# Performance work log

Hardware: AMD Instinct MI355X
Metric: run time of the kernel (lower is better)

The kernel has to match this reference:

```python
import jax, jax.numpy as jnp
import numpy as np

HEADS = 2
NEG_SLOPE = 0.2

def _seg_softmax(alpha, dst, n):
    # numerically-stable softmax over edges grouped by destination node (PyG softmax)
    m = jax.ops.segment_max(alpha, dst, num_segments=n)
    m = jax.lax.stop_gradient(jnp.where(jnp.isfinite(m), m, 0.0))
    e = jnp.exp(alpha - m[dst])
    s = jax.ops.segment_sum(e, dst, num_segments=n)
    return e / (s[dst] + 1e-16)

def _han_layer(xo, xa, e_oo, e_oa, e_ao, Wo, bo, Wa, ba, asrc, adst, Wk, bk, q):
    No, Na = xo.shape[0], xa.shape[0]
    C = Wo.shape[1]
    D = C // HEADS
    h = {'object': (xo @ Wo + bo).reshape(No, HEADS, D),
         'attribute': (xa @ Wa + ba).reshape(Na, HEADS, D)}
    n = {'object': No, 'attribute': Na}
    edge_types = [('object', 'object', e_oo), ('object', 'attribute', e_oa),
                  ('attribute', 'object', e_ao)]
    outs = {'object': [], 'attribute': []}
    for i, (st, dt, e) in enumerate(edge_types):
        src, dst = e[0], e[1]
        # per-edge attention logits [E, H]
        a = (h[st] * asrc[i]).sum(-1)[src] + (h[dt] * adst[i]).sum(-1)[dst]
        a = jax.nn.leaky_relu(a, NEG_SLOPE)
        a = _seg_softmax(a, dst, n[dt])
        msg = (h[st][src] * a[..., None]).reshape(-1, C)  # [E, C]
        outs[dt].append(jax.nn.relu(jax.ops.segment_sum(msg, dst, num_segments=n[dt])))
    res = {}
    for nt, xs in outs.items():
        o = jnp.stack(xs)  # [M, N, C] over metapaths
        score = (q * jnp.tanh(o @ Wk + bk).mean(axis=1)).sum(-1)  # [M]
        w = jax.nn.softmax(score, axis=0)
        res[nt] = jnp.einsum('m,mnc->nc', w, o)
    return res


def setup_inputs() -> dict:
    key = jax.random.key(0)
    ks = jax.random.split(key, 40)
    No, Na, E, C, H = 100000, 50000, 500000, 128, 2
    D = C // H
    def rn(k, shape, scale):
        return jax.random.normal(k, shape, jnp.float32) * scale
    inp = {}
    inp['x_object'] = rn(ks[0], (No, C), 1.0)
    inp['x_attribute'] = rn(ks[1], (Na, C), 1.0)
    inp['e_oo'] = jax.random.randint(ks[2], (2, E), 0, No)
    inp['e_oa'] = jnp.stack([jax.random.randint(ks[3], (E,), 0, No),
                             jax.random.randint(ks[4], (E,), 0, Na)])
    inp['e_ao'] = jnp.stack([jax.random.randint(ks[5], (E,), 0, Na),
                             jax.random.randint(ks[6], (E,), 0, No)])
    s = 1.0 / float(np.sqrt(C))
    for L, off in (('1', 7), ('2', 16)):
        inp['Wo' + L] = rn(ks[off], (C, C), s)
        inp['bo' + L] = jnp.zeros((C,), jnp.float32)
        inp['Wa' + L] = rn(ks[off + 1], (C, C), s)
        inp['ba' + L] = jnp.zeros((C,), jnp.float32)
        inp['asrc' + L] = rn(ks[off + 2], (3, H, D), s)
        inp['adst' + L] = rn(ks[off + 3], (3, H, D), s)
        inp['Wk' + L] = rn(ks[off + 4], (C, C), s)
        inp['bk' + L] = jnp.zeros((C,), jnp.float32)
        inp['q' + L] = rn(ks[off + 5], (C,), s)
    inp['Wl1'] = rn(ks[30], (C, 256), s)
    inp['bl1'] = jnp.zeros((256,), jnp.float32)
    inp['Wl2'] = rn(ks[31], (256, 128), 1.0 / float(np.sqrt(256)))
    inp['bl2'] = jnp.zeros((128,), jnp.float32)
    inp['Wl3'] = rn(ks[32], (128, 8), 1.0 / float(np.sqrt(128)))
    inp['bl3'] = jnp.zeros((8,), jnp.float32)
    return inp


def reference(x_object, x_attribute, e_oo, e_oa, e_ao,
              Wo1, bo1, Wa1, ba1, asrc1, adst1, Wk1, bk1, q1,
              Wo2, bo2, Wa2, ba2, asrc2, adst2, Wk2, bk2, q2,
              Wl1, bl1, Wl2, bl2, Wl3, bl3):
    h = _han_layer(x_object, x_attribute, e_oo, e_oa, e_ao,
                   Wo1, bo1, Wa1, ba1, asrc1, adst1, Wk1, bk1, q1)
    h = _han_layer(h['object'], h['attribute'], e_oo, e_oa, e_ao,
                   Wo2, bo2, Wa2, ba2, asrc2, adst2, Wk2, bk2, q2)
    x = h['object'] @ Wl1 + bl1
    x = x @ Wl2 + bl2
    x = x @ Wl3 + bl3
    return jax.nn.sigmoid(x)
```

## Files before the change

kernel.cpp:

```cpp
#include <hip/hip_runtime.h>
#include <hip/hip_bf16.h>
#include <math.h>

#define CDIM 128
typedef unsigned short u16;
typedef unsigned int u32;
typedef short bf16x8 __attribute__((ext_vector_type(8)));
typedef float f32x4 __attribute__((ext_vector_type(4)));

__device__ __forceinline__ float bf2f(__hip_bfloat16 h) { return __bfloat162float(h); }
__device__ __forceinline__ u16 f2bfbits(float f) {
  __hip_bfloat16 h = __float2bfloat16(f);
  u16 u;
  __builtin_memcpy(&u, &h, 2);
  return u;
}
__device__ __forceinline__ float bfbits2f(u16 b) { return __uint_as_float((u32)b << 16); }
__device__ __forceinline__ float lrelu(float v) { return v > 0.f ? v : 0.2f * v; }
__device__ __forceinline__ float lo_bf(u32 v) { return __uint_as_float(v << 16); }
__device__ __forceinline__ float hi_bf(u32 v) { return __uint_as_float(v & 0xffff0000u); }
__device__ __forceinline__ u32 pack_bf(float a, float b) {
  return (u32)f2bfbits(a) | ((u32)f2bfbits(b) << 16);
}

__global__ void detect_kernel(const u16* __restrict__ p, int nwords, int* __restrict__ flag) {
  int i = blockIdx.x * blockDim.x + threadIdx.x;
  if (i >= nwords) return;
  int ex = (p[i] >> 7) & 0xFF;
  if (ex >= 0xC0) atomicOr(flag, 1);
}

struct CvtJob { const void* src; float* dst; int n; };
struct CvtJobs24 { CvtJob j[24]; };
__global__ void cvt_batch_kernel(CvtJobs24 jobs, const int* __restrict__ flag) {
  CvtJob jb = jobs.j[blockIdx.y];
  int i = blockIdx.x * blockDim.x + threadIdx.x;
  if (i >= jb.n) return;
  if (*flag) jb.dst[i] = ((const float*)jb.src)[i];
  else jb.dst[i] = bf2f(((const __hip_bfloat16*)jb.src)[i]);
}

__global__ void fill_out_kernel(void* __restrict__ out, float v, int n,
                                const int* __restrict__ flag) {
  int i = blockIdx.x * blockDim.x + threadIdx.x;
  if (i >= n) return;
  if (*flag) ((float*)out)[i] = v;
  else ((__hip_bfloat16*)out)[i] = __float2bfloat16(v);
}

struct RepackJobs { const float* src[6]; u16* dst[6]; };
__global__ void repack_w_kernel(RepackJobs jobs) {
  const float* W = jobs.src[blockIdx.y];
  u16* Wf = jobs.dst[blockIdx.y];
  int idx = blockIdx.x * 256 + threadIdx.x;
  int j = idx & 7, lane = (idx >> 3) & 63, kc = (idx >> 9) & 3, nt = idx >> 11;
  int k = kc * 32 + ((lane >> 4) & 3) * 8 + j;
  int n = nt * 16 + (lane & 15);
  Wf[idx] = f2bfbits(W[k * 128 + n]);
}

struct CsrJobs {
  const int* src[3]; const int* dst[3];
  int* deg[3]; int* cur[3]; int* bsum[3]; int* offs[3]; int* adj[3];
  int Nd[3]; int E;
};
__global__ void deg_batch_kernel(CsrJobs c) {
  int y = blockIdx.y;
  int e = blockIdx.x * blockDim.x + threadIdx.x;
  if (e < c.E) atomicAdd(&c.deg[y][c.dst[y][e]], 1);
}
__global__ void scanp_batch_kernel(CsrJobs c) {
  int y = blockIdx.y, N = c.Nd[y];
  __shared__ int red[256];
  int t = threadIdx.x;
  int base = blockIdx.x * 1024 + t * 4;
  int s = 0;
#pragma unroll
  for (int j = 0; j < 4; ++j) if (base + j < N) s += c.deg[y][base + j];
  red[t] = s;
  __syncthreads();
  for (int o = 128; o; o >>= 1) {
    if (t < o) red[t] += red[t + o];
    __syncthreads();
  }
  if (t == 0) c.bsum[y][blockIdx.x] = red[0];
}
__global__ void scanb_batch_kernel(CsrJobs c) {
  int y = threadIdx.x;
  if (y >= 3) return;
  int nb = (c.Nd[y] + 1023) / 1024;
  int run = 0;
  for (int i = 0; i < nb; ++i) { int v = c.bsum[y][i]; c.bsum[y][i] = run; run += v; }
  c.offs[y][c.Nd[y]] = c.E;
}
__global__ void scanf_batch_kernel(CsrJobs c) {
  int y = blockIdx.y, N = c.Nd[y];
  __shared__ int lds[256];
  int t = threadIdx.x;
  int base = blockIdx.x * 1024 + t * 4;
  int v0 = (base + 0 < N) ? c.deg[y][base + 0] : 0;
  int v1 = (base + 1 < N) ? c.deg[y][base + 1] : 0;
  int v2 = (base + 2 < N) ? c.deg[y][base + 2] : 0;
  int v3 = (base + 3 < N) ? c.deg[y][base + 3] : 0;
  int tsum = v0 + v1 + v2 + v3;
  lds[t] = tsum;
  __syncthreads();
  for (int o = 1; o < 256; o <<= 1) {
    int x = (t >= o) ? lds[t - o] : 0;
    __syncthreads();
    lds[t] += x;
    __syncthreads();
  }
  int excl = lds[t] - tsum + c.bsum[y][blockIdx.x];
  int e0 = excl, e1 = excl + v0, e2 = excl + v0 + v1, e3 = excl + v0 + v1 + v2;
  if (base + 0 < N) { c.offs[y][base + 0] = e0; c.cur[y][base + 0] = e0; }
  if (base + 1 < N) { c.offs[y][base + 1] = e1; c.cur[y][base + 1] = e1; }
  if (base + 2 < N) { c.offs[y][base + 2] = e2; c.cur[y][base + 2] = e2; }
  if (base + 3 < N) { c.offs[y][base + 3] = e3; c.cur[y][base + 3] = e3; }
}
__global__ void fill_batch_kernel(CsrJobs c, int R) {
  int y = blockIdx.y;
  int e = blockIdx.x * blockDim.x + threadIdx.x;
  if (e >= c.E) return;
  int Nd = c.Nd[y];
  int range = (Nd + R - 1) / R;
  int lo = blockIdx.z * range;
  int d = c.dst[y][e];
  if (d < lo || d >= lo + range) return;
  int p = atomicAdd(&c.cur[y][d], 1);
  c.adj[y][p] = c.src[y][e];
}

struct GemmJob {
  const void* X; const void* X2; const float* W2;
  const u16* Wf; const float* bias;
  const float* av[4]; float* od[4]; int K;
  u16* out; int M; int mode;
};
struct GemmJobs2 { GemmJob j[2]; };
__global__ __launch_bounds__(256, 4) void gemm_mfma_kernel(
    GemmJobs2 g, const int* __restrict__ flag, int nb0)
{
  int jbi = ((int)blockIdx.x >= nb0) ? 1 : 0;
  GemmJob jb = g.j[jbi];
  int bx = jbi ? (int)blockIdx.x - nb0 : (int)blockIdx.x;
  int M = jb.M;
  __shared__ u16 Cs[64][136];
  int wave = threadIdx.x >> 6, lane = threadIdx.x & 63;
  int row0 = bx * 64 + wave * 16;
  int m = lane & 15, ko = (lane >> 4) * 8, rq = lane >> 4;
  bool wact = row0 < M;
  if (wact) {
    int r = row0 + m; if (r >= M) r = M - 1;
    bf16x8 a[4];
    if (jb.mode == 1 && *flag) {
      const float* af = (const float*)jb.X + (size_t)r * 128 + ko;
#pragma unroll
      for (int c = 0; c < 4; ++c) {
        float4 x = *(const float4*)(af + c * 32);
        float4 y = *(const float4*)(af + c * 32 + 4);
        bf16x8 tv;
        tv[0] = (short)f2bfbits(x.x); tv[1] = (short)f2bfbits(x.y);
        tv[2] = (short)f2bfbits(x.z); tv[3] = (short)f2bfbits(x.w);
        tv[4] = (short)f2bfbits(y.x); tv[5] = (short)f2bfbits(y.y);
        tv[6] = (short)f2bfbits(y.z); tv[7] = (short)f2bfbits(y.w);
        a[c] = tv;
      }
    } else if (jb.mode == 2) {
      float w0 = jb.W2[0], w1 = jb.W2[1];
      const u16* g1 = (const u16*)jb.X + (size_t)r * 128 + ko;
      const u16* g2 = (const u16*)jb.X2 + (size_t)r * 128 + ko;
#pragma unroll
      for (int c = 0; c < 4; ++c) {
        bf16x8 x1 = *(const bf16x8*)(g1 + c * 32);
        bf16x8 x2 = *(const bf16x8*)(g2 + c * 32);
        bf16x8 tv;
#pragma unroll
        for (int k = 0; k < 8; ++k)
          tv[k] = (short)f2bfbits(w0 * bfbits2f((u16)x1[k]) + w1 * bfbits2f((u16)x2[k]));
        a[c] = tv;
      }
    } else {
      const u16* ab = (const u16*)jb.X + (size_t)r * 128 + ko;
#pragma unroll
      for (int c = 0; c < 4; ++c) a[c] = *(const bf16x8*)(ab + c * 32);
    }
    f32x4 acc[8];
#pragma unroll
    for (int nt = 0; nt < 8; ++nt) acc[nt] = (f32x4){0.f, 0.f, 0.f, 0.f};
#pragma unroll
    for (int c = 0; c < 4; ++c) {
      bf16x8 b[8];
#pragma unroll
      for (int nt = 0; nt < 8; ++nt)
        b[nt] = *(const bf16x8*)(jb.Wf + ((nt * 4 + c) * 64 + lane) * 8);
#pragma unroll
      for (int nt = 0; nt < 8; ++nt)
        acc[nt] = __builtin_amdgcn_mfma_f32_16x16x32_bf16(a[c], b[nt], acc[nt], 0, 0, 0);
    }
#pragma unroll
    for (int nt = 0; nt < 8; ++nt) {
      float bv = jb.bias[nt * 16 + m];
#pragma unroll
      for (int reg = 0; reg < 4; ++reg) acc[nt][reg] += bv;
    }
#pragma unroll
    for (int nt = 0; nt < 8; ++nt) {
      int col = nt * 16 + m;
#pragma unroll
      for (int reg = 0; reg < 4; ++reg)
        Cs[wave * 16 + rq * 4 + reg][col] = f2bfbits(acc[nt][reg]);
    }
    for (int k = 0; k < jb.K; ++k) {
      const float* avk = jb.av[k];
      float* odk = jb.od[k];
      float am[8];
#pragma unroll
      for (int nt = 0; nt < 8; ++nt) am[nt] = avk[nt * 16 + m];
#pragma unroll
      for (int reg = 0; reg < 4; ++reg) {
        float p0 = 0.f, p1 = 0.f;
#pragma unroll
        for (int nt = 0; nt < 4; ++nt) p0 = fmaf(acc[nt][reg], am[nt], p0);
#pragma unroll
        for (int nt = 4; nt < 8; ++nt) p1 = fmaf(acc[nt][reg], am[nt], p1);
#pragma unroll
        for (int msk = 1; msk < 16; msk <<= 1) {
          p0 += __shfl_xor(p0, msk);
          p1 += __shfl_xor(p1, msk);
        }
        if (m == 0) {
          int row = row0 + rq * 4 + reg;
          if (row < M) { odk[row * 2] = p0; odk[row * 2 + 1] = p1; }
        }
      }
    }
  }
  __syncthreads();
  int t = threadIdx.x;
#pragma unroll
  for (int kk = 0; kk < 4; ++kk) {
    int idx = t + kk * 256;
    int rowl = idx >> 4, c16 = idx & 15;
    int grow = bx * 64 + rowl;
    if (grow < M) {
      uint4 v = *(const uint4*)&Cs[rowl][c16 * 8];
      *(uint4*)((u16*)jb.out + (size_t)grow * 128 + c16 * 8) = v;
    }
  }
}

__global__ __launch_bounds__(256) void tanhsum_mfma_kernel(
    const u16* __restrict__ A0, const u16* __restrict__ A1,
    const u16* __restrict__ Wf, const float* __restrict__ bias,
    float* __restrict__ score, int M)
{
  const u16* A = blockIdx.y ? A1 : A0;
  float* sc = score + blockIdx.y * 128;
  __shared__ float sred[4][128];
  int wave = threadIdx.x >> 6, lane = threadIdx.x & 63;
  int m = lane & 15, ko = (lane >> 4) * 8, rq = lane >> 4;
  float colsum[8];
#pragma unroll
  for (int nt = 0; nt < 8; ++nt) colsum[nt] = 0.f;
  for (int row0 = blockIdx.x * 64 + wave * 16; row0 < M; row0 += gridDim.x * 64) {
    int r = row0 + m; if (r >= M) r = M - 1;
    const u16* arow = A + (size_t)r * 128 + ko;
    bf16x8 a[4];
#pragma unroll
    for (int c = 0; c < 4; ++c) a[c] = *(const bf16x8*)(arow + c * 32);
    f32x4 acc[8];
#pragma unroll
    for (int nt = 0; nt < 8; ++nt) acc[nt] = (f32x4){0.f, 0.f, 0.f, 0.f};
#pragma unroll
    for (int c = 0; c < 4; ++c) {
#pragma unroll
      for (int nt = 0; nt < 8; ++nt) {
        bf16x8 b = *(const bf16x8*)(Wf + ((nt * 4 + c) * 64 + lane) * 8);
        acc[nt] = __builtin_amdgcn_mfma_f32_16x16x32_bf16(a[c], b, acc[nt], 0, 0, 0);
      }
    }
#pragma unroll
    for (int nt = 0; nt < 8; ++nt) {
      float bv = bias[nt * 16 + m];
#pragma unroll
      for (int reg = 0; reg < 4; ++reg) {
        int row = row0 + rq * 4 + reg;
        if (row < M) colsum[nt] += tanhf(acc[nt][reg] + bv);
      }
    }
  }
#pragma unroll
  for (int nt = 0; nt < 8; ++nt) {
    colsum[nt] += __shfl_xor(colsum[nt], 16);
    colsum[nt] += __shfl_xor(colsum[nt], 32);
  }
  if (lane < 16) {
#pragma unroll
    for (int nt = 0; nt < 8; ++nt) sred[wave][nt * 16 + lane] = colsum[nt];
  }
  __syncthreads();
  int t = threadIdx.x;
  if (t < 128) {
    float tot = sred[0][t] + sred[1][t] + sred[2][t] + sred[3][t];
    atomicAdd(&sc[t], tot);
  }
}

__global__ void sem_w_kernel(const float* __restrict__ score, const float* __restrict__ q,
                             float invN, float* __restrict__ W2) {
  int t = threadIdx.x;
  float s0 = 0.f, s1 = 0.f;
  for (int c = t; c < 128; c += 64) {
    float qc = q[c];
    s0 += qc * score[c];
    s1 += qc * score[128 + c];
  }
#pragma unroll
  for (int o = 32; o; o >>= 1) {
    s0 += __shfl_xor(s0, o);
    s1 += __shfl_xor(s1, o);
  }
  if (t == 0) {
    s0 *= invN; s1 *= invN;
    float mx = fmaxf(s0, s1);
    float e0 = expf(s0 - mx), e1 = expf(s1 - mx);
    float inv = 1.f / (e0 + e1);
    W2[0] = e0 * inv;
    W2[1] = e1 * inv;
  }
}

struct GatherJob {
  const int* offs; const int* adj;
  const float* ss; const float* sd;
  float* ew;
  const u16* Hs; u16* out; int Nd;
};
struct GatherJobs3 { GatherJob j[3]; };
__global__ __launch_bounds__(256) void node_gather_b_kernel(GatherJobs3 g, int nb0, int nb01)
{
  int bx = blockIdx.x;
  int jbi = bx < nb0 ? 0 : (bx < nb01 ? 1 : 2);
  int bl = jbi == 0 ? bx : (jbi == 1 ? bx - nb0 : bx - nb01);
  GatherJob jb = g.j[jbi];
  int lane = threadIdx.x & 63;
  int grp = lane >> 4, sl = lane & 15;
  int wid = bl * 4 + (threadIdx.x >> 6);
  int node = wid * 4 + grp;
  bool act = node < jb.Nd;
  int beg = 0, end = 0;
  float2 sdp = make_float2(0.f, 0.f);
  if (act) {
    beg = jb.offs[node];
    end = jb.offs[node + 1];
    sdp = ((const float2*)jb.sd)[node];
  }
  int deg = end - beg;
  const float2* ss2 = (const float2*)jb.ss;
  float2* ew2 = (float2*)jb.ew;
  const uint4* H4 = (const uint4*)jb.Hs;
  bool hi2 = sl >= 8;
  int base = grp * 16;
  float a[8];
#pragma unroll
  for (int j = 0; j < 8; ++j) a[j] = 0.f;
  float invh;
  if (__all(deg <= 16)) {
    int adjreg = 0;
    if (sl < deg) adjreg = jb.adj[beg + sl];
    int sidx[8];
#pragma unroll
    for (int j = 0; j < 8; ++j) sidx[j] = __shfl(adjreg, base + j);
    float2 ssp = make_float2(0.f, 0.f);
    if (sl < deg) ssp = ss2[adjreg];
    uint4 v[8];
#pragma unroll
    for (int j = 0; j < 8; ++j)
      if (j < deg) v[j] = H4[(size_t)sidx[j] * 16 + sl];
    float e0r = 0.f, e1r = 0.f;
    if (sl < deg) {
      e0r = expf(lrelu(ssp.x + sdp.x));
      e1r = expf(lrelu(ssp.y + sdp.y));
    }
    float s0 = e0r, s1 = e1r;
#pragma unroll
    for (int o = 1; o < 16; o <<= 1) {
      s0 += __shfl_xor(s0, o);
      s1 += __shfl_xor(s1, o);
    }
    invh = 1.f / ((hi2 ? s1 : s0) + 1e-16f);
#pragma unroll
    for (int j = 0; j < 8; ++j) {
      float wl = __shfl(e0r, base + j);
      float wh = __shfl(e1r, base + j);
      if (j < deg) {
        float w = hi2 ? wh : wl;
        a[0] = fmaf(lo_bf(v[j].x), w, a[0]);
        a[1] = fmaf(hi_bf(v[j].x), w, a[1]);
        a[2] = fmaf(lo_bf(v[j].y), w, a[2]);
        a[3] = fmaf(hi_bf(v[j].y), w, a[3]);
        a[4] = fmaf(lo_bf(v[j].z), w, a[4]);
        a[5] = fmaf(hi_bf(v[j].z), w, a[5]);
        a[6] = fmaf(lo_bf(v[j].w), w, a[6]);
        a[7] = fmaf(hi_bf(v[j].w), w, a[7]);
      }
    }
    if (__any(deg > 8)) {
#pragma unroll
      for (int j = 0; j < 8; ++j) {
        int s2 = __shfl(adjreg, base + 8 + j);
        float wl = __shfl(e0r, base + 8 + j);
        float wh = __shfl(e1r, base + 8 + j);
        if (8 + j < deg) {
          uint4 vv = H4[(size_t)s2 * 16 + sl];
          float w = hi2 ? wh : wl;
          a[0] = fmaf(lo_bf(vv.x), w, a[0]);
          a[1] = fmaf(hi_bf(vv.x), w, a[1]);
          a[2] = fmaf(lo_bf(vv.y), w, a[2]);
          a[3] = fmaf(hi_bf(vv.y), w, a[3]);
          a[4] = fmaf(lo_bf(vv.z), w, a[4]);
          a[5] = fmaf(hi_bf(vv.z), w, a[5]);
          a[6] = fmaf(lo_bf(vv.w), w, a[6]);
          a[7] = fmaf(hi_bf(vv.w), w, a[7]);
        }
      }
    }
  } else {
    float s0 = 0.f, s1 = 0.f;
    for (int e = beg + sl; e < end; e += 16) {
      int s = jb.adj[e];
      float2 ssp = ss2[s];
      float f0 = expf(lrelu(ssp.x + sdp.x));
      float f1 = expf(lrelu(ssp.y + sdp.y));
      ew2[e] = make_float2(f0, f1);
      s0 += f0;
      s1 += f1;
    }
#pragma unroll
    for (int o = 1; o < 16; o <<= 1) {
      s0 += __shfl_xor(s0, o);
      s1 += __shfl_xor(s1, o);
    }
    invh = 1.f / ((hi2 ? s1 : s0) + 1e-16f);
    for (int eb = beg; eb < end; eb += 4) {
      int eA[4]; uint4 v[4]; float w[4];
#pragma unroll
      for (int j = 0; j < 4; ++j) eA[j] = (eb + j < end) ? eb + j : end - 1;
#pragma unroll
      for (int j = 0; j < 4; ++j) v[j] = H4[(size_t)jb.adj[eA[j]] * 16 + sl];
#pragma unroll
      for (int j = 0; j < 4; ++j) {
        float2 p = ew2[eA[j]];
        w[j] = (eb + j < end) ? (hi2 ? p.y : p.x) : 0.f;
      }
#pragma unroll
      for (int j = 0; j < 4; ++j) {
        a[0] = fmaf(lo_bf(v[j].x), w[j], a[0]);
        a[1] = fmaf(hi_bf(v[j].x), w[j], a[1]);
        a[2] = fmaf(lo_bf(v[j].y), w[j], a[2]);
        a[3] = fmaf(hi_bf(v[j].y), w[j], a[3]);
        a[4] = fmaf(lo_bf(v[j].z), w[j], a[4]);
        a[5] = fmaf(hi_bf(v[j].z), w[j], a[5]);
        a[6] = fmaf(lo_bf(v[j].w), w[j], a[6]);
        a[7] = fmaf(hi_bf(v[j].w), w[j], a[7]);
      }
    }
  }
  if (act) {
    uint4 o;
    o.x = pack_bf(fmaxf(a[0] * invh, 0.f), fmaxf(a[1] * invh, 0.f));
    o.y = pack_bf(fmaxf(a[2] * invh, 0.f), fmaxf(a[3] * invh, 0.f));
    o.z = pack_bf(fmaxf(a[4] * invh, 0.f), fmaxf(a[5] * invh, 0.f));
    o.w = pack_bf(fmaxf(a[6] * invh, 0.f), fmaxf(a[7] * invh, 0.f));
    ((uint4*)jb.out)[(size_t)node * 16 + sl] = o;
  }
}

__global__ void fold1_kernel(const float* __restrict__ Wl1, const float* __restrict__ bl1,
                             const float* __restrict__ Wl2, const float* __restrict__ bl2,
                             float* __restrict__ WT1, float* __restrict__ TB) {
  int idx = blockIdx.x * blockDim.x + threadIdx.x;
  if (idx < 128 * 128) {
    int m = idx >> 7, n = idx & 127;
    float acc = 0.f;
    for (int k = 0; k < 256; ++k) acc = fmaf(Wl1[m * 256 + k], Wl2[k * 128 + n], acc);
    WT1[idx] = acc;
  } else if (idx < 128 * 128 + 128) {
    int n = idx - 128 * 128;
    float acc = bl2[n];
    for (int k = 0; k < 256; ++k) acc = fmaf(bl1[k], Wl2[k * 128 + n], acc);
    TB[n] = acc;
  }
}
__global__ void fold2_kernel(const float* __restrict__ WT1, const float* __restrict__ TB,
                             const float* __restrict__ Wl3, const float* __restrict__ bl3,
                             float* __restrict__ WC, float* __restrict__ BC) {
  int idx = blockIdx.x * blockDim.x + threadIdx.x;
  if (idx < 128 * 8) {
    int m = idx >> 3, j = idx & 7;
    float acc = 0.f;
    for (int k = 0; k < 128; ++k) acc = fmaf(WT1[m * 128 + k], Wl3[k * 8 + j], acc);
    WC[idx] = acc;
  } else if (idx < 128 * 8 + 8) {
    int j = idx - 128 * 8;
    float acc = bl3[j];
    for (int k = 0; k < 128; ++k) acc = fmaf(TB[k], Wl3[k * 8 + j], acc);
    BC[j] = acc;
  }
}

__global__ __launch_bounds__(256) void final_mlp_kernel(
    const u16* __restrict__ X1, const u16* __restrict__ X2,
    const float* __restrict__ W2, const int* __restrict__ flag,
    const float* __restrict__ Wc, const float* __restrict__ bc,
    void* __restrict__ out, int M) {
  __shared__ float Xs[32][130];
  int rb = blockIdx.x * 32;
  int t = threadIdx.x;
  float w0 = W2[0], w1 = W2[1];
  for (int i = t; i < 32 * 64; i += 256) {
    int r = i >> 6, c2 = i & 63;
    int gr = rb + r;
    u32 v1 = 0, v2 = 0;
    if (gr < M) {
      v1 = ((const u32*)X1)[(size_t)gr * 64 + c2];
      v2 = ((const u32*)X2)[(size_t)gr * 64 + c2];
    }
    Xs[r][c2 * 2] = w0 * lo_bf(v1) + w1 * lo_bf(v2);
    Xs[r][c2 * 2 + 1] = w0 * hi_bf(v1) + w1 * hi_bf(v2);
  }
  __syncthreads();
  int r = t >> 3, j = t & 7;
  int gr = rb + r;
  if (gr >= M) return;
  float acc = bc[j];
#pragma unroll 4
  for (int c = 0; c < 128; ++c) acc = fmaf(Xs[r][c], Wc[c * 8 + j], acc);
  float v = 1.f / (1.f + expf(-acc));
  if (*flag) ((float*)out)[(size_t)gr * 8 + j] = v;
  else ((__hip_bfloat16*)out)[(size_t)gr * 8 + j] = __float2bfloat16(v);
}

extern "C" void kernel_launch(void* const* d_in, const int* in_sizes, int n_in,
                              void* d_out, int out_size, void* d_ws, size_t ws_size,
                              hipStream_t stream) {
  const int No = in_sizes[0] / CDIM;
  const int Na = in_sizes[1] / CDIM;
  const int E = in_sizes[2] / 2;
  const int NM = No > Na ? No : Na;

  char* base = (char*)d_ws;
  size_t off = 0;
  auto alloc = [&](size_t bytes) -> void* {
    off = (off + 255) & ~(size_t)255;
    void* p = base + off;
    off += bytes;
    return p;
  };

  int* FLAG = (int*)alloc(4);
  u16* G1b = (u16*)alloc((size_t)No * CDIM * 2);
  u16* XAb = (u16*)alloc((size_t)Na * CDIM * 2);
  u16* HOb = (u16*)alloc((size_t)No * CDIM * 2);
  u16* HAb = (u16*)alloc((size_t)Na * CDIM * 2);
  u16* G2b = (u16*)alloc((size_t)No * CDIM * 2);
  float* OD0 = (float*)alloc((size_t)No * 2 * 4);
  float* OD1 = (float*)alloc((size_t)No * 2 * 4);
  float* OD2 = (float*)alloc((size_t)No * 2 * 4);
  float* OD3 = (float*)alloc((size_t)No * 2 * 4);
  float* AD0 = (float*)alloc((size_t)Na * 2 * 4);
  float* AD1 = (float*)alloc((size_t)Na * 2 * 4);
  float* EW0 = (float*)alloc((size_t)E * 2 * 4);
  float* EW1 = (float*)alloc((size_t)E * 2 * 4);
  float* EW2 = (float*)alloc((size_t)E * 2 * 4);
  int* DEG3 = (int*)alloc((size_t)NM * 3 * 4);
  float* SCORE = (float*)alloc(512 * 4);
  float* SEMW = (float*)alloc(4 * 4);
  float* WT1 = (float*)alloc(128 * 128 * 4);
  float* TB = (float*)alloc(128 * 4);
  float* WC = (float*)alloc(128 * 8 * 4);
  float* BC = (float*)alloc(8 * 4);
  int* OFFS_OO = (int*)alloc((size_t)(No + 1) * 4);
  int* OFFS_OA = (int*)alloc((size_t)(Na + 1) * 4);
  int* OFFS_AO = (int*)alloc((size_t)(No + 1) * 4);
  int* ADJ_OO = (int*)alloc((size_t)E * 4);
  int* ADJ_OA = (int*)alloc((size_t)E * 4);
  int* ADJ_AO = (int*)alloc((size_t)E * 4);
  int* CUR3 = (int*)alloc((size_t)NM * 3 * 4);
  int* BSUM3 = (int*)alloc(3 * 128 * 4);
  u16* WF[6];
  for (int i = 0; i < 6; ++i) WF[i] = (u16*)alloc(16384 * 2);
  float* F[29];
  for (int i = 5; i < 29; ++i) F[i] = (float*)alloc((size_t)in_sizes[i] * 4);

  hipMemsetAsync(FLAG, 0, 4, stream);
  detect_kernel<<<64, 256, 0, stream>>>((const u16*)d_in[0], 16384, FLAG);

  if (off > ws_size) {
    fill_out_kernel<<<(out_size + 255) / 256, 256, 0, stream>>>(d_out, 0.25f, out_size, FLAG);
    return;
  }

  {
    CvtJobs24 jobs;
    int maxn = 0;
    for (int i = 5; i < 29; ++i) {
      jobs.j[i - 5].src = d_in[i];
      jobs.j[i - 5].dst = F[i];
      jobs.j[i - 5].n = in_sizes[i];
      if (in_sizes[i] > maxn) maxn = in_sizes[i];
    }
    dim3 g((maxn + 255) / 256, 24);
    cvt_batch_kernel<<<g, 256, 0, stream>>>(jobs, FLAG);
  }

  {
    RepackJobs rj;
    const int widx[6] = { 5, 7, 11, 14, 16, 20 };
    for (int i = 0; i < 6; ++i) { rj.src[i] = F[widx[i]]; rj.dst[i] = WF[i]; }
    dim3 g(64, 6);
    repack_w_kernel<<<g, 256, 0, stream>>>(rj);
  }

  {
    CsrJobs c;
    const int* EOO = (const int*)d_in[2];
    const int* EOA = (const int*)d_in[3];
    const int* EAO = (const int*)d_in[4];
    c.src[0] = EOO; c.dst[0] = EOO + E; c.Nd[0] = No; c.offs[0] = OFFS_OO; c.adj[0] = ADJ_OO;
    c.src[1] = EOA; c.dst[1] = EOA + E; c.Nd[1] = Na; c.offs[1] = OFFS_OA; c.adj[1] = ADJ_OA;
    c.src[2] = EAO; c.dst[2] = EAO + E; c.Nd[2] = No; c.offs[2] = OFFS_AO; c.adj[2] = ADJ_AO;
    for (int i = 0; i < 3; ++i) {
      c.deg[i] = DEG3 + (size_t)i * NM;
      c.cur[i] = CUR3 + (size_t)i * NM;
      c.bsum[i] = BSUM3 + i * 128;
    }
    c.E = E;
    size_t zlen = (size_t)((char*)(SEMW + 4) - (char*)DEG3);
    hipMemsetAsync(DEG3, 0, zlen, stream);
    int nbmax = (NM + 1023) / 1024;
    deg_batch_kernel<<<dim3((E + 255) / 256, 3), 256, 0, stream>>>(c);
    scanp_batch_kernel<<<dim3(nbmax, 3), 256, 0, stream>>>(c);
    scanb_batch_kernel<<<1, 64, 0, stream>>>(c);
    scanf_batch_kernel<<<dim3(nbmax, 3), 256, 0, stream>>>(c);
    fill_batch_kernel<<<dim3((E + 255) / 256, 3, 4), 256, 0, stream>>>(c, 4);
  }

  const int nb0 = (No + 63) / 64;
  const int nb1 = (Na + 63) / 64;

  auto run_layer = [&](int L, const void* XO, const void* XO2, const float* W2in,
                       const void* XA, int mode0,
                       const float* bo, const float* ba,
                       const float* av, const float* ad, const float* bk,
                       const float* q) {
    u16* WFo = WF[L * 3 + 0];
    u16* WFa = WF[L * 3 + 1];
    u16* WFk = WF[L * 3 + 2];
    float* SC = SCORE + L * 256;
    GemmJobs2 gj;
    gj.j[0].X = XO; gj.j[0].X2 = XO2; gj.j[0].W2 = W2in;
    gj.j[0].Wf = WFo; gj.j[0].bias = bo; gj.j[0].mode = mode0;
    gj.j[0].av[0] = av + 0;   gj.j[0].od[0] = OD0;
    gj.j[0].av[1] = ad + 0;   gj.j[0].od[1] = OD1;
    gj.j[0].av[2] = av + 128; gj.j[0].od[2] = OD2;
    gj.j[0].av[3] = ad + 256; gj.j[0].od[3] = OD3;
    gj.j[0].K = 4; gj.j[0].out = HOb; gj.j[0].M = No;
    gj.j[1].X = XA; gj.j[1].X2 = nullptr; gj.j[1].W2 = nullptr;
    gj.j[1].Wf = WFa; gj.j[1].bias = ba; gj.j[1].mode = (L == 0) ? 1 : 0;
    gj.j[1].av[0] = av + 256; gj.j[1].od[0] = AD0;
    gj.j[1].av[1] = ad + 128; gj.j[1].od[1] = AD1;
    gj.j[1].av[2] = nullptr;  gj.j[1].od[2] = nullptr;
    gj.j[1].av[3] = nullptr;  gj.j[1].od[3] = nullptr;
    gj.j[1].K = L == 0 ? 2 : 1; gj.j[1].out = HAb; gj.j[1].M = Na;
    gemm_mfma_kernel<<<nb0 + nb1, 256, 0, stream>>>(gj, FLAG, nb0);

    GatherJobs3 ga;
    ga.j[0] = { OFFS_OO, ADJ_OO, OD0, OD1, EW0, HOb, G1b, No };
    int c0 = (No + 15) / 16, c1, c2;
    if (L == 0) {
      ga.j[1] = { OFFS_OA, ADJ_OA, OD2, AD1, EW1, HOb, XAb, Na };
      ga.j[2] = { OFFS_AO, ADJ_AO, AD0, OD3, EW2, HAb, G2b, No };
      c1 = (Na + 15) / 16;
      c2 = (No + 15) / 16;
    } else {
      ga.j[1] = { OFFS_AO, ADJ_AO, AD0, OD3, EW2, HAb, G2b, No };
      ga.j[2] = ga.j[1];
      c1 = (No + 15) / 16;
      c2 = 0;
    }
    node_gather_b_kernel<<<c0 + c1 + c2, 256, 0, stream>>>(ga, c0, c0 + c1);

    tanhsum_mfma_kernel<<<dim3(512, 2), 256, 0, stream>>>(G1b, G2b, WFk, bk, SC, No);
    sem_w_kernel<<<1, 64, 0, stream>>>(SC, q, 1.f / (float)No, SEMW + L * 2);
  };

  run_layer(0, d_in[0], nullptr, nullptr, d_in[1], 1,
            F[6], F[8], F[9], F[10], F[12], F[13]);
  run_layer(1, G1b, G2b, SEMW, XAb, 2,
            F[15], F[17], F[18], F[19], F[21], F[22]);

  fold1_kernel<<<(128 * 128 + 128 + 255) / 256, 256, 0, stream>>>(F[23], F[24], F[25], F[26], WT1, TB);
  fold2_kernel<<<(128 * 8 + 8 + 255) / 256, 256, 0, stream>>>(WT1, TB, F[27], F[28], WC, BC);

  final_mlp_kernel<<<(No + 31) / 32, 256, 0, stream>>>(G1b, G2b, SEMW + 2, FLAG, WC, BC, d_out, No);
}
```

Measured before the change: 672.4 us.

## Stage packed weights in LDS and replicate them across blocks in global memory

The repacked bf16 weight matrix is now written in 8 copies, and each block picks a copy by block index. At kernel start the block copies its 32KB copy into shared memory, and the MFMA loops then read B fragments from LDS instead of global memory. The A-row loads move before the barrier so they overlap with the weight staging. The intent is to cut L2/global traffic and contention on one hot weight buffer. In exchange it adds 32KB of LDS per block, which may lower occupancy under launch_bounds(256,4), plus an extra barrier and the larger repack.

```diff
diff --git a/kernel.cpp b/kernel.cpp
--- a/kernel.cpp
+++ b/kernel.cpp
@@ -22,6 +22,9 @@
 __device__ __forceinline__ u32 pack_bf(float a, float b) {
   return (u32)f2bfbits(a) | ((u32)f2bfbits(b) << 16);
 }
+
+#define WREP 8
+#define WFSZ 16384
 
 __global__ void detect_kernel(const u16* __restrict__ p, int nwords, int* __restrict__ flag) {
   int i = blockIdx.x * blockDim.x + threadIdx.x;
@@ -51,7 +54,7 @@
 struct RepackJobs { const float* src[6]; u16* dst[6]; };
 __global__ void repack_w_kernel(RepackJobs jobs) {
   const float* W = jobs.src[blockIdx.y];
-  u16* Wf = jobs.dst[blockIdx.y];
+  u16* Wf = jobs.dst[blockIdx.y] + ((size_t)blockIdx.z << 14);
   int idx = blockIdx.x * 256 + threadIdx.x;
   int j = idx & 7, lane = (idx >> 3) & 63, kc = (idx >> 9) & 3, nt = idx >> 11;
   int k = kc * 32 + ((lane >> 4) & 3) * 8 + j;
@@ -145,46 +148,55 @@
   GemmJob jb = g.j[jbi];
   int bx = jbi ? (int)blockIdx.x - nb0 : (int)blockIdx.x;
   int M = jb.M;
+  __shared__ __align__(16) u16 Bs[WFSZ];
   __shared__ u16 Cs[64][136];
-  int wave = threadIdx.x >> 6, lane = threadIdx.x & 63;
+  int t = threadIdx.x;
+  int wave = t >> 6, lane = t & 63;
   int row0 = bx * 64 + wave * 16;
   int m = lane & 15, ko = (lane >> 4) * 8, rq = lane >> 4;
   bool wact = row0 < M;
+  int r = row0 + m; if (r >= M) r = M - 1;
+  bf16x8 a[4];
+  if (jb.mode == 1 && *flag) {
+    const float* af = (const float*)jb.X + (size_t)r * 128 + ko;
+#pragma unroll
+    for (int c = 0; c < 4; ++c) {
+      float4 x = *(const float4*)(af + c * 32);
+      float4 y = *(const float4*)(af + c * 32 + 4);
+      bf16x8 tv;
+      tv[0] = (short)f2bfbits(x.x); tv[1] = (short)f2bfbits(x.y);
+      tv[2] = (short)f2bfbits(x.z); tv[3] = (short)f2bfbits(x.w);
+      tv[4] = (short)f2bfbits(y.x); tv[5] = (short)f2bfbits(y.y);
+      tv[6] = (short)f2bfbits(y.z); tv[7] = (short)f2bfbits(y.w);
+      a[c] = tv;
+    }
+  } else if (jb.mode == 2) {
+    float w0 = jb.W2[0], w1 = jb.W2[1];
+    const u16* g1 = (const u16*)jb.X + (size_t)r * 128 + ko;
+    const u16* g2 = (const u16*)jb.X2 + (size_t)r * 128 + ko;
+#pragma unroll
+    for (int c = 0; c < 4; ++c) {
+      bf16x8 x1 = *(const bf16x8*)(g1 + c * 32);
+      bf16x8 x2 = *(const bf16x8*)(g2 + c * 32);
+      bf16x8 tv;
+#pragma unroll
+      for (int k = 0; k < 8; ++k)
+        tv[k] = (short)f2bfbits(w0 * bfbits2f((u16)x1[k]) + w1 * bfbits2f((u16)x2[k]));
+      a[c] = tv;
+    }
+  } else {
+    const u16* ab = (const u16*)jb.X + (size_t)r * 128 + ko;
+#pragma unroll
+    for (int c = 0; c < 4; ++c) a[c] = *(const bf16x8*)(ab + c * 32);
+  }
+  {
+    const uint4* wfg = (const uint4*)(jb.Wf + ((size_t)(bx & (WREP - 1)) << 14));
+    uint4* bs4 = (uint4*)Bs;
+#pragma unroll
+    for (int i = 0; i < 8; ++i) bs4[t + i * 256] = wfg[t + i * 256];
+  }
+  __syncthreads();
   if (wact) {
-    int r = row0 + m; if (r >= M) r = M - 1;
-    bf16x8 a[4];
-    if (jb.mode == 1 && *flag) {
-      const float* af = (const float*)jb.X + (size_t)r * 128 + ko;
-#pragma unroll
-      for (int c = 0; c < 4; ++c) {
-        float4 x = *(const float4*)(af + c * 32);
-        float4 y = *(const float4*)(af + c * 32 + 4);
-        bf16x8 tv;
-        tv[0] = (short)f2bfbits(x.x); tv[1] = (short)f2bfbits(x.y);
-        tv[2] = (short)f2bfbits(x.z); tv[3] = (short)f2bfbits(x.w);
-        tv[4] = (short)f2bfbits(y.x); tv[5] = (short)f2bfbits(y.y);
-        tv[6] = (short)f2bfbits(y.z); tv[7] = (short)f2bfbits(y.w);
-        a[c] = tv;
-      }
-    } else if (jb.mode == 2) {
-      float w0 = jb.W2[0], w1 = jb.W2[1];
-      const u16* g1 = (const u16*)jb.X + (size_t)r * 128 + ko;
-      const u16* g2 = (const u16*)jb.X2 + (size_t)r * 128 + ko;
-#pragma unroll
-      for (int c = 0; c < 4; ++c) {
-        bf16x8 x1 = *(const bf16x8*)(g1 + c * 32);
-        bf16x8 x2 = *(const bf16x8*)(g2 + c * 32);
-        bf16x8 tv;
-#pragma unroll
-        for (int k = 0; k < 8; ++k)
-          tv[k] = (short)f2bfbits(w0 * bfbits2f((u16)x1[k]) + w1 * bfbits2f((u16)x2[k]));
-        a[c] = tv;
-      }
-    } else {
-      const u16* ab = (const u16*)jb.X + (size_t)r * 128 + ko;
-#pragma unroll
-      for (int c = 0; c < 4; ++c) a[c] = *(const bf16x8*)(ab + c * 32);
-    }
     f32x4 acc[8];
 #pragma unroll
     for (int nt = 0; nt < 8; ++nt) acc[nt] = (f32x4){0.f, 0.f, 0.f, 0.f};
@@ -193,7 +205,7 @@
       bf16x8 b[8];
 #pragma unroll
       for (int nt = 0; nt < 8; ++nt)
-        b[nt] = *(const bf16x8*)(jb.Wf + ((nt * 4 + c) * 64 + lane) * 8);
+        b[nt] = *(const bf16x8*)(Bs + ((nt * 4 + c) * 64 + lane) * 8);
 #pragma unroll
       for (int nt = 0; nt < 8; ++nt)
         acc[nt] = __builtin_amdgcn_mfma_f32_16x16x32_bf16(a[c], b[nt], acc[nt], 0, 0, 0);
@@ -237,7 +249,6 @@
     }
   }
   __syncthreads();
-  int t = threadIdx.x;
 #pragma unroll
   for (int kk = 0; kk < 4; ++kk) {
     int idx = t + kk * 256;
@@ -257,9 +268,18 @@
 {
   const u16* A = blockIdx.y ? A1 : A0;
   float* sc = score + blockIdx.y * 128;
+  __shared__ __align__(16) u16 Bs[WFSZ];
   __shared__ float sred[4][128];
-  int wave = threadIdx.x >> 6, lane = threadIdx.x & 63;
+  int t = threadIdx.x;
+  int wave = t >> 6, lane = t & 63;
   int m = lane & 15, ko = (lane >> 4) * 8, rq = lane >> 4;
+  {
+    const uint4* wfg = (const uint4*)(Wf + ((size_t)(blockIdx.x & (WREP - 1)) << 14));
+    uint4* bs4 = (uint4*)Bs;
+#pragma unroll
+    for (int i = 0; i < 8; ++i) bs4[t + i * 256] = wfg[t + i * 256];
+  }
+  __syncthreads();
   float colsum[8];
 #pragma unroll
   for (int nt = 0; nt < 8; ++nt) colsum[nt] = 0.f;
@@ -274,11 +294,13 @@
     for (int nt = 0; nt < 8; ++nt) acc[nt] = (f32x4){0.f, 0.f, 0.f, 0.f};
 #pragma unroll
     for (int c = 0; c < 4; ++c) {
-#pragma unroll
-      for (int nt = 0; nt < 8; ++nt) {
-        bf16x8 b = *(const bf16x8*)(Wf + ((nt * 4 + c) * 64 + lane) * 8);
-        acc[nt] = __builtin_amdgcn_mfma_f32_16x16x32_bf16(a[c], b, acc[nt], 0, 0, 0);
-      }
+      bf16x8 b[8];
+#pragma unroll
+      for (int nt = 0; nt < 8; ++nt)
+        b[nt] = *(const bf16x8*)(Bs + ((nt * 4 + c) * 64 + lane) * 8);
+#pragma unroll
+      for (int nt = 0; nt < 8; ++nt)
+        acc[nt] = __builtin_amdgcn_mfma_f32_16x16x32_bf16(a[c], b[nt], acc[nt], 0, 0, 0);
     }
 #pragma unroll
     for (int nt = 0; nt < 8; ++nt) {
@@ -300,7 +322,6 @@
     for (int nt = 0; nt < 8; ++nt) sred[wave][nt * 16 + lane] = colsum[nt];
   }
   __syncthreads();
-  int t = threadIdx.x;
   if (t < 128) {
     float tot = sred[0][t] + sred[1][t] + sred[2][t] + sred[3][t];
     atomicAdd(&sc[t], tot);
@@ -590,7 +611,7 @@
   int* CUR3 = (int*)alloc((size_t)NM * 3 * 4);
   int* BSUM3 = (int*)alloc(3 * 128 * 4);
   u16* WF[6];
-  for (int i = 0; i < 6; ++i) WF[i] = (u16*)alloc(16384 * 2);
+  for (int i = 0; i < 6; ++i) WF[i] = (u16*)alloc((size_t)WFSZ * WREP * 2);
   float* F[29];
   for (int i = 5; i < 29; ++i) F[i] = (float*)alloc((size_t)in_sizes[i] * 4);
 
@@ -619,7 +640,7 @@
     RepackJobs rj;
     const int widx[6] = { 5, 7, 11, 14, 16, 20 };
     for (int i = 0; i < 6; ++i) { rj.src[i] = F[widx[i]]; rj.dst[i] = WF[i]; }
-    dim3 g(64, 6);
+    dim3 g(64, 6, WREP);
     repack_w_kernel<<<g, 256, 0, stream>>>(rj);
   }
 
```

Result: no change. 679.4 us (+1.0%).
